# Optimization experiments

Measured on AMD Instinct MI355X. Metric: run time of the kernel, lower is better.

Reference implementation:

```python
import jax, jax.numpy as jnp
import numpy as np

N, E, IN_DIM, HID, HEADS, LAYERS, NTYPES, NGRAPH = 50000, 600000, 64, 128, 8, 3, 10, 500
C = HID // HEADS
NEG_SLOPE = 0.2
EPS = 1e-5


def setup_inputs() -> dict:
    key = jax.random.key(0)
    ks = jax.random.split(key, 24)
    inp = {
        "x": jax.random.normal(ks[0], (N, IN_DIM), jnp.float32),
        "edge_index": jax.random.randint(ks[1], (2, E), 0, N),
        "node_types": jax.random.randint(ks[2], (N,), 0, NTYPES),
        "batch": jnp.sort(jax.random.randint(ks[3], (N,), 0, NGRAPH)),
        # node embedding linear
        "emb_W": jax.random.normal(ks[4], (IN_DIM, HID), jnp.float32) / np.sqrt(IN_DIM),
        "emb_b": jnp.zeros((HID,), jnp.float32),
        "ntype_emb": jax.random.normal(ks[5], (NTYPES, HID), jnp.float32) * 0.02,
        # stacked GAT layer params
        "gat_W": jax.random.normal(ks[6], (LAYERS, HID, HID), jnp.float32) / np.sqrt(HID),
        "att_src": jax.random.normal(ks[7], (LAYERS, HEADS, C), jnp.float32) * 0.1,
        "att_dst": jax.random.normal(ks[8], (LAYERS, HEADS, C), jnp.float32) * 0.1,
        "gat_b": jnp.zeros((LAYERS, HID), jnp.float32),
        "ln_g": jnp.ones((LAYERS, HID), jnp.float32),
        "ln_b": jnp.zeros((LAYERS, HID), jnp.float32),
        # global attention MLP
        "ga_W1": jax.random.normal(ks[9], (HID, HID), jnp.float32) / np.sqrt(HID),
        "ga_b1": jnp.zeros((HID,), jnp.float32),
        "ga_W2": jax.random.normal(ks[10], (HID, 1), jnp.float32) / np.sqrt(HID),
        "ga_b2": jnp.zeros((1,), jnp.float32),
        # graph classifier head
        "cls_W1": jax.random.normal(ks[11], (HID, HID), jnp.float32) / np.sqrt(HID),
        "cls_b1": jnp.zeros((HID,), jnp.float32),
        "cls_W2": jax.random.normal(ks[12], (HID, 1), jnp.float32) / np.sqrt(HID),
        "cls_b2": jnp.zeros((1,), jnp.float32),
    }
    return inp


def _layer_norm(h, g, b):
    mu = jnp.mean(h, axis=-1, keepdims=True)
    var = jnp.mean(jnp.square(h - mu), axis=-1, keepdims=True)
    return (h - mu) * jax.lax.rsqrt(var + EPS) * g + b


def _gat_layer(h, src, dst, W, a_src, a_dst, bias):
    # h: [N, HID] -> per-head projection [N, H, C]
    hp = (h @ W).reshape(N, HEADS, C)
    alpha_s = jnp.sum(hp * a_src, axis=-1)  # [N, H]
    alpha_d = jnp.sum(hp * a_dst, axis=-1)  # [N, H]
    e = jax.nn.leaky_relu(alpha_s[src] + alpha_d[dst], NEG_SLOPE)  # [E', H]
    # segment softmax over incoming edges of each destination node
    m = jax.ops.segment_max(e, dst, num_segments=N)
    ex = jnp.exp(e - m[dst])
    s = jax.ops.segment_sum(ex, dst, num_segments=N)
    alpha = ex / s[dst]  # every node has a self-loop, so s > 0
    msg = hp[src] * alpha[:, :, None]  # [E', H, C]
    out = jax.ops.segment_sum(msg, dst, num_segments=N)  # [N, H, C]
    return out.reshape(N, HID) + bias


def reference(x, edge_index, node_types, batch, emb_W, emb_b, ntype_emb,
              gat_W, att_src, att_dst, gat_b, ln_g, ln_b,
              ga_W1, ga_b1, ga_W2, ga_b2, cls_W1, cls_b1, cls_W2, cls_b2):
    # self-loops (PyG GATConv add_self_loops=True)
    loop = jnp.arange(N)
    src = jnp.concatenate([edge_index[0], loop])
    dst = jnp.concatenate([edge_index[1], loop])

    h = x @ emb_W + emb_b
    h = h + ntype_emb[node_types]

    for l in range(LAYERS):
        h_prev = h
        h = _gat_layer(h, src, dst, gat_W[l], att_src[l], att_dst[l], gat_b[l])
        h = _layer_norm(h, ln_g[l], ln_b[l])
        h = jax.nn.relu(h + h_prev)

    # global attention pooling: softmax over all nodes (dim 0, as in source)
    scores = jnp.tanh(h @ ga_W1 + ga_b1) @ ga_W2 + ga_b2  # [N, 1]
    attw = jax.nn.softmax(scores, axis=0)
    h_graph = jnp.sum(h * attw, axis=0)  # [HID]

    # global mean pool per graph
    sums = jax.ops.segment_sum(h, batch, num_segments=NGRAPH)  # [G, HID]
    cnts = jax.ops.segment_sum(jnp.ones((N, 1), h.dtype), batch, num_segments=NGRAPH)
    mean_pool = sums / jnp.maximum(cnts, 1.0)

    hg = h_graph + mean_pool  # broadcast [HID] + [G, HID]

    # graph classifier head (features_batch=None path), squeeze(-1)
    out = jax.nn.relu(hg @ cls_W1 + cls_b1) @ cls_W2 + cls_b2
    return out.squeeze(-1)  # [G]
```

## Files before the change

### kernel.cpp

```cpp
#include <hip/hip_runtime.h>
#include <hip/hip_bf16.h>
#include <math.h>

#define HID 128
#define HEADS 8
#define INDIM 64

typedef _Float16 f16x8 __attribute__((ext_vector_type(8)));
typedef _Float16 f16x4 __attribute__((ext_vector_type(4)));
typedef _Float16 f16x2 __attribute__((ext_vector_type(2)));
typedef float f32x4 __attribute__((ext_vector_type(4)));

__device__ __forceinline__ float fast_tanh(float x) {
    return 1.f - 2.f / (__expf(2.f * x) + 1.f);
}

#if defined(__has_builtin)
#if __has_builtin(__builtin_amdgcn_fdot2)
#define HAVE_FDOT2 1
#endif
#endif

__global__ void prologue_kernel(const int* __restrict__ ei, int* __restrict__ deg,
                                const float* __restrict__ x, _Float16* __restrict__ x16,
                                const float* __restrict__ emb_W, const float* __restrict__ gat_W,
                                const float* __restrict__ ga_W1, _Float16* __restrict__ wt_emb,
                                _Float16* __restrict__ wt_gat, _Float16* __restrict__ wt_ga1,
                                const int* __restrict__ batch, int* __restrict__ gstart,
                                float* __restrict__ hgZ,
                                int E, int EE, int N, int G, int XT4) {
    int i = blockIdx.x * blockDim.x + threadIdx.x;
    if (i < XT4) {
        float4 v = ((const float4*)x)[i];
        f16x4 o; o[0] = (_Float16)v.x; o[1] = (_Float16)v.y; o[2] = (_Float16)v.z; o[3] = (_Float16)v.w;
        *(f16x4*)&x16[4 * i] = o;
    }
    if (i < EE) {
        int dst = (i < E) ? ei[E + i] : (i - E);
        atomicAdd(&deg[dst], 1);
    }
    if (i < 8192) {
        int k = i >> 7, n = i & 127;
        wt_emb[n * 64 + k] = (_Float16)emb_W[i];
    } else if (i < 8192 + 49152) {
        int j = i - 8192;
        int l = j >> 14, r = j & 16383;
        int k = r >> 7, n = r & 127;
        wt_gat[l * 16384 + n * 128 + k] = (_Float16)gat_W[j];
    } else if (i < 73728) {
        int j = i - 57344;
        int k = j >> 7, n = j & 127;
        wt_ga1[n * 128 + k] = (_Float16)ga_W1[j];
    } else if (i < 73728 + 129) {
        hgZ[i - 73728] = 0.f;
    }
    if (i >= 100000 && i - 100000 <= G) {
        int g = i - 100000;
        int lo = 0, hi = N;
        while (lo < hi) {
            int mid = (lo + hi) >> 1;
            if (batch[mid] < g) lo = mid + 1; else hi = mid;
        }
        gstart[g] = lo;
    }
}

__global__ void block_sum_kernel(const int* __restrict__ deg, int* __restrict__ partials, int N) {
    __shared__ int sdata[4];
    int t = threadIdx.x;
    int i = blockIdx.x * 256 + t;
    int v = (i < N) ? deg[i] : 0;
#pragma unroll
    for (int m = 32; m >= 1; m >>= 1) v += __shfl_xor(v, m, 64);
    if ((t & 63) == 0) sdata[t >> 6] = v;
    __syncthreads();
    if (t == 0) partials[blockIdx.x] = sdata[0] + sdata[1] + sdata[2] + sdata[3];
}

__global__ void scan_partials_kernel(int* __restrict__ partials, int nb) {
    int lane = threadIdx.x;
    int carry = 0;
    for (int base = 0; base < nb; base += 64) {
        int i = base + lane;
        int v = (i < nb) ? partials[i] : 0;
        int orig = v;
#pragma unroll
        for (int off = 1; off < 64; off <<= 1) {
            int x = __shfl_up(v, off, 64);
            if (lane >= off) v += x;
        }
        if (i < nb) partials[i] = v - orig + carry;
        carry += __shfl(v, 63, 64);
    }
}

__global__ void rowptr_kernel(const int* __restrict__ deg, const int* __restrict__ partials,
                              int* __restrict__ rowptr, int* __restrict__ woff, int N, int EE) {
    __shared__ int tmp[256];
    int t = threadIdx.x;
    int i = blockIdx.x * 256 + t;
    int v = (i < N) ? deg[i] : 0;
    tmp[t] = v;
    __syncthreads();
#pragma unroll
    for (int off = 1; off < 256; off <<= 1) {
        int x = (t >= off) ? tmp[t - off] : 0;
        __syncthreads();
        tmp[t] += x;
        __syncthreads();
    }
    int excl = tmp[t] - v + partials[blockIdx.x];
    if (i < N) { rowptr[i] = excl; woff[i] = excl; }
    if (blockIdx.x == 0 && t == 0) rowptr[N] = EE;
}

__global__ void scatter_kernel(const int* __restrict__ ei, int* __restrict__ woff,
                               int* __restrict__ esrc, int E, int EE) {
    int e = blockIdx.x * blockDim.x + threadIdx.x;
    if (e >= EE) return;
    int src, dst;
    if (e < E) { src = ei[e]; dst = ei[E + e]; } else { src = dst = e - E; }
    int slot = atomicAdd(&woff[dst], 1);
    esrc[slot] = src;
}

__global__ __launch_bounds__(256) void mfma_proj_kernel(
    int mode, int K, int N,
    const _Float16* __restrict__ A16, const _Float16* __restrict__ Wt,
    const float* __restrict__ bias, const float* __restrict__ nemb,
    const int* __restrict__ ntypes, _Float16* __restrict__ h16out,
    const float* __restrict__ asrc, const float* __restrict__ adst,
    _Float16* __restrict__ hp_out, float* __restrict__ als, float* __restrict__ ald,
    const float* __restrict__ w2, const float* __restrict__ b2,
    float* __restrict__ escore)
{
    __shared__ _Float16 w_lds[128 * 136];
    __shared__ _Float16 a_lds[64 * 136];
    int t = threadIdx.x;
    int KP = K + 8;
    int K8 = K >> 3;

    for (int i = t; i < 128 * K8; i += 256) {
        int row = i / K8, c8 = i - row * K8;
        *(f16x8*)&w_lds[row * KP + 8 * c8] = *(const f16x8*)&Wt[(size_t)row * K + 8 * c8];
    }

    int lane = t & 63, wv = t >> 6;
    int l15 = lane & 15, quad = lane >> 4;

    for (int tile = 0; tile < 2; ++tile) {
        int n0 = blockIdx.x * 128 + tile * 64;
        if (n0 >= N) break;
        __syncthreads();
        for (int i = t; i < 64 * K8; i += 256) {
            int row = i / K8, c8 = i - row * K8;
            f16x8 v = {};
            if (n0 + row < N) v = *(const f16x8*)&A16[(size_t)(n0 + row) * K + 8 * c8];
            *(f16x8*)&a_lds[row * KP + 8 * c8] = v;
        }
        __syncthreads();

        f32x4 acc[8];
#pragma unroll
        for (int c = 0; c < 8; ++c) acc[c] = (f32x4){0.f, 0.f, 0.f, 0.f};

        int ksteps = K >> 5;
        for (int kk = 0; kk < ksteps; ++kk) {
            f16x8 af = *(const f16x8*)&a_lds[(wv * 16 + l15) * KP + kk * 32 + quad * 8];
#pragma unroll
            for (int c = 0; c < 8; ++c) {
                f16x8 bf = *(const f16x8*)&w_lds[(c * 16 + l15) * KP + kk * 32 + quad * 8];
                acc[c] = __builtin_amdgcn_mfma_f32_16x16x32_f16(af, bf, acc[c], 0, 0, 0);
            }
        }

        if (mode == 0) {
            float bv[8];
#pragma unroll
            for (int c = 0; c < 8; ++c) bv[c] = bias[c * 16 + l15];
            __syncthreads();
#pragma unroll
            for (int r = 0; r < 4; ++r) {
                int n = n0 + wv * 16 + quad * 4 + r;
                int nt = (n < N) ? ntypes[n] : 0;
#pragma unroll
                for (int c = 0; c < 8; ++c)
                    a_lds[(wv * 16 + quad * 4 + r) * 136 + c * 16 + l15] =
                        (_Float16)(acc[c][r] + bv[c] + nemb[nt * HID + c * 16 + l15]);
            }
            __syncthreads();
            for (int i = t; i < 64 * 16; i += 256) {
                int row = i >> 4, c8 = i & 15;
                int n = n0 + row;
                if (n < N) *(f16x8*)&h16out[(size_t)n * HID + 8 * c8] = *(const f16x8*)&a_lds[row * 136 + 8 * c8];
            }
        } else if (mode == 1) {
            __syncthreads();
#pragma unroll
            for (int c = 0; c < 8; ++c)
#pragma unroll
                for (int r = 0; r < 4; ++r)
                    a_lds[(wv * 16 + quad * 4 + r) * 136 + c * 16 + l15] = (_Float16)acc[c][r];
            __syncthreads();
            for (int i = t; i < 64 * 16; i += 256) {
                int row = i >> 4, c8 = i & 15;
                int n = n0 + row;
                if (n < N) *(f16x8*)&hp_out[(size_t)n * HID + 8 * c8] = *(const f16x8*)&a_lds[row * 136 + 8 * c8];
            }
            for (int task = t; task < 512; task += 256) {
                int row = task >> 3, hd = task & 7;
                int n = n0 + row;
                if (n >= N) continue;
                f16x8 v0 = *(const f16x8*)&a_lds[row * 136 + hd * 16];
                f16x8 v1 = *(const f16x8*)&a_lds[row * 136 + hd * 16 + 8];
                float va = 0.f, vd = 0.f;
#pragma unroll
                for (int j = 0; j < 8; ++j) {
                    va += (float)v0[j] * asrc[hd * 16 + j] + (float)v1[j] * asrc[hd * 16 + 8 + j];
                    vd += (float)v0[j] * adst[hd * 16 + j] + (float)v1[j] * adst[hd * 16 + 8 + j];
                }
                als[n * HEADS + hd] = va;
                ald[n * HEADS + hd] = vd;
            }
        } else {
            float b2v = b2[0];
            float treg[4] = {0.f, 0.f, 0.f, 0.f};
#pragma unroll
            for (int c = 0; c < 8; ++c) {
                float b1v = bias[c * 16 + l15];
                float w2v = w2[c * 16 + l15];
#pragma unroll
                for (int r = 0; r < 4; ++r)
                    treg[r] += fast_tanh(acc[c][r] + b1v) * w2v;
            }
#pragma unroll
            for (int r = 0; r < 4; ++r) {
                float v = treg[r];
#pragma unroll
                for (int m = 8; m >= 1; m >>= 1) v += __shfl_xor(v, m, 64);
                if (l15 == 0) {
                    int n = n0 + wv * 16 + quad * 4 + r;
                    if (n < N) escore[n] = __expf(v + b2v);
                }
            }
        }
    }
}

__global__ void gat_aggregate_kernel(const int* __restrict__ rowptr, const int* __restrict__ esrc,
                                     const float* __restrict__ als, const float* __restrict__ ald,
                                     const _Float16* __restrict__ hp16, const float* __restrict__ gb,
                                     const float* __restrict__ lg, const float* __restrict__ lb,
                                     _Float16* __restrict__ h16, int N) {
    int wave = threadIdx.x >> 6;
    int lane = threadIdx.x & 63;
    int n = blockIdx.x * 4 + wave;
    if (n >= N) return;
    int esub = lane >> 4;
    int cg = lane & 15;
    int hd = cg >> 1;
    float adv = ald[n * HEADS + hd];
    int row = rowptr[n], end = rowptr[n + 1];
    int last = end - 1;
    float acc[8] = {0.f, 0.f, 0.f, 0.f, 0.f, 0.f, 0.f, 0.f};
    float sw = 0.f;
    for (int base = row; base < end; base += 16) {
        int iA = base + esub;
        int iB = iA + 4, iC = iA + 8, iD = iA + 12;
        int cA = iA <= last ? iA : last;
        int cB = iB <= last ? iB : last;
        int cC = iC <= last ? iC : last;
        int cD = iD <= last ? iD : last;
        int sA = esrc[cA], sB = esrc[cB], sC = esrc[cC], sD = esrc[cD];
        f16x8 pA = *(const f16x8*)&hp16[(size_t)sA * HID + cg * 8];
        f16x8 pB = *(const f16x8*)&hp16[(size_t)sB * HID + cg * 8];
        f16x8 pC = *(const f16x8*)&hp16[(size_t)sC * HID + cg * 8];
        f16x8 pD = *(const f16x8*)&hp16[(size_t)sD * HID + cg * 8];
        float aA = als[sA * HEADS + hd];
        float aB = als[sB * HEADS + hd];
        float aC = als[sC * HEADS + hd];
        float aD = als[sD * HEADS + hd];
        float lA = aA + adv; lA = lA > 0.f ? lA : 0.2f * lA;
        float lB = aB + adv; lB = lB > 0.f ? lB : 0.2f * lB;
        float lC = aC + adv; lC = lC > 0.f ? lC : 0.2f * lC;
        float lD = aD + adv; lD = lD > 0.f ? lD : 0.2f * lD;
        float wA = __expf(lA) * ((iA < end) ? 1.f : 0.f);
        float wB = __expf(lB) * ((iB < end) ? 1.f : 0.f);
        float wC = __expf(lC) * ((iC < end) ? 1.f : 0.f);
        float wD = __expf(lD) * ((iD < end) ? 1.f : 0.f);
        sw += (wA + wB) + (wC + wD);
#ifdef HAVE_FDOT2
        f16x2 wAB; wAB[0] = (_Float16)wA; wAB[1] = (_Float16)wB;
        f16x2 wCD; wCD[0] = (_Float16)wC; wCD[1] = (_Float16)wD;
#pragma unroll
        for (int j = 0; j < 8; ++j) {
            f16x2 prAB; prAB[0] = pA[j]; prAB[1] = pB[j];
            f16x2 prCD; prCD[0] = pC[j]; prCD[1] = pD[j];
            acc[j] = __builtin_amdgcn_fdot2(prAB, wAB, acc[j], false);
            acc[j] = __builtin_amdgcn_fdot2(prCD, wCD, acc[j], false);
        }
#else
#pragma unroll
        for (int j = 0; j < 8; ++j)
            acc[j] += wA * (float)pA[j] + wB * (float)pB[j]
                    + wC * (float)pC[j] + wD * (float)pD[j];
#endif
    }
#pragma unroll
    for (int m = 16; m <= 32; m <<= 1) {
        sw += __shfl_xor(sw, m, 64);
#pragma unroll
        for (int j = 0; j < 8; ++j) acc[j] += __shfl_xor(acc[j], m, 64);
    }
    float inv_sw = 1.f / sw;
    float4 g0 = ((const float4*)(gb + cg * 8))[0];
    float4 g1 = ((const float4*)(gb + cg * 8))[1];
    float v[8];
    v[0] = acc[0] * inv_sw + g0.x; v[1] = acc[1] * inv_sw + g0.y;
    v[2] = acc[2] * inv_sw + g0.z; v[3] = acc[3] * inv_sw + g0.w;
    v[4] = acc[4] * inv_sw + g1.x; v[5] = acc[5] * inv_sw + g1.y;
    v[6] = acc[6] * inv_sw + g1.z; v[7] = acc[7] * inv_sw + g1.w;
    float s = 0.f;
#pragma unroll
    for (int j = 0; j < 8; ++j) s += v[j];
#pragma unroll
    for (int m = 32; m >= 1; m >>= 1) s += __shfl_xor(s, m, 64);
    float mu = s * (1.f / 512.f);
    float d[8], sq = 0.f;
#pragma unroll
    for (int j = 0; j < 8; ++j) { d[j] = v[j] - mu; sq += d[j] * d[j]; }
#pragma unroll
    for (int m = 32; m >= 1; m >>= 1) sq += __shfl_xor(sq, m, 64);
    float inv = rsqrtf(sq * (1.f / 512.f) + 1e-5f);
    float4 lg0 = ((const float4*)(lg + cg * 8))[0];
    float4 lg1 = ((const float4*)(lg + cg * 8))[1];
    float4 lb0 = ((const float4*)(lb + cg * 8))[0];
    float4 lb1 = ((const float4*)(lb + cg * 8))[1];
    float lgv[8] = {lg0.x, lg0.y, lg0.z, lg0.w, lg1.x, lg1.y, lg1.z, lg1.w};
    float lbv[8] = {lb0.x, lb0.y, lb0.z, lb0.w, lb1.x, lb1.y, lb1.z, lb1.w};
    f16x8 hold = *(const f16x8*)&h16[(size_t)n * HID + cg * 8];
    f16x8 hnew;
#pragma unroll
    for (int j = 0; j < 8; ++j) {
        float r = d[j] * inv * lgv[j] + lbv[j] + (float)hold[j];
        hnew[j] = (_Float16)(r > 0.f ? r : 0.f);
    }
    if (esub == 0) *(f16x8*)&h16[(size_t)n * HID + cg * 8] = hnew;
}

__global__ void pool_graph_kernel(const _Float16* __restrict__ h16, const float* __restrict__ escore,
                                  const int* __restrict__ gstart, float* __restrict__ sums,
                                  float* __restrict__ cnts, float* __restrict__ hgZ, int G) {
    int g = blockIdx.x;
    int t = threadIdx.x;
    int c = t & 127, grp = t >> 7;
    int s = gstart[g], e = gstart[g + 1];
    float msum = 0.f, asum = 0.f, z = 0.f;
    for (int n = s + grp; n < e; n += 4) {
        float hv = (float)h16[(size_t)n * HID + c];
        float es = escore[n];
        msum += hv;
        asum += es * hv;
        if (c == 0) z += es;
    }
    __shared__ float sm[4][HID];
    __shared__ float sa[4][HID];
    __shared__ float sz[4];
    sm[grp][c] = msum;
    sa[grp][c] = asum;
    if (c == 0) sz[grp] = z;
    __syncthreads();
    if (t < HID) {
        float m = sm[0][t] + sm[1][t] + sm[2][t] + sm[3][t];
        float a = sa[0][t] + sa[1][t] + sa[2][t] + sa[3][t];
        sums[(size_t)g * HID + t] = m;
        atomicAdd(&hgZ[t], a);
    } else if (t == HID) {
        cnts[g] = (float)(e - s);
        atomicAdd(&hgZ[HID], sz[0] + sz[1] + sz[2] + sz[3]);
    }
}

__global__ void head_kernel(const float* __restrict__ hgZ, const float* __restrict__ sums,
                            const float* __restrict__ cnts, const float* __restrict__ W1,
                            const float* __restrict__ b1, const float* __restrict__ W2,
                            const float* __restrict__ b2, float* __restrict__ out, int G) {
    int g = blockIdx.x;
    int t = threadIdx.x;
    __shared__ float hr[HID];
    __shared__ float part[2];
    float Z = hgZ[HID];
    float cnt = cnts[g];
    cnt = cnt > 1.f ? cnt : 1.f;
    hr[t] = hgZ[t] / Z + sums[(size_t)g * HID + t] / cnt;
    __syncthreads();
    float acc = b1[t];
#pragma unroll 8
    for (int k = 0; k < HID; ++k) acc += hr[k] * W1[k * HID + t];
    acc = acc > 0.f ? acc : 0.f;
    float v = acc * W2[t];
#pragma unroll
    for (int m = 32; m >= 1; m >>= 1) v += __shfl_xor(v, m, 64);
    if ((t & 63) == 0) part[t >> 6] = v;
    __syncthreads();
    if (t == 0) out[g] = part[0] + part[1] + b2[0];
}

extern "C" void kernel_launch(void* const* d_in, const int* in_sizes, int n_in,
                              void* d_out, int out_size, void* d_ws, size_t ws_size,
                              hipStream_t stream) {
    const float* x        = (const float*)d_in[0];
    const int*   ei       = (const int*)d_in[1];
    const int*   ntypes   = (const int*)d_in[2];
    const int*   batch    = (const int*)d_in[3];
    const float* emb_W    = (const float*)d_in[4];
    const float* emb_b    = (const float*)d_in[5];
    const float* nemb     = (const float*)d_in[6];
    const float* gat_W    = (const float*)d_in[7];
    const float* att_src  = (const float*)d_in[8];
    const float* att_dst  = (const float*)d_in[9];
    const float* gat_b    = (const float*)d_in[10];
    const float* ln_g     = (const float*)d_in[11];
    const float* ln_b     = (const float*)d_in[12];
    const float* ga_W1    = (const float*)d_in[13];
    const float* ga_b1    = (const float*)d_in[14];
    const float* ga_W2    = (const float*)d_in[15];
    const float* ga_b2    = (const float*)d_in[16];
    const float* cls_W1   = (const float*)d_in[17];
    const float* cls_b1   = (const float*)d_in[18];
    const float* cls_W2   = (const float*)d_in[19];
    const float* cls_b2   = (const float*)d_in[20];
    float* out = (float*)d_out;

    const int N  = in_sizes[2];
    const int E  = in_sizes[1] / 2;
    const int EE = E + N;
    const int G  = out_size;
    const int NB = (N + 255) / 256;
    const int XT4 = N * INDIM / 4;

    float* ws      = (float*)d_ws;
    float* als     = ws;
    float* ald     = als + (size_t)N * HEADS;
    float* escore  = ald + (size_t)N * HEADS;
    float* sums    = escore + N;
    float* cnts    = sums + (size_t)G * HID;
    float* hgZ     = cnts + G;
    _Float16* h16  = (_Float16*)(hgZ + HID + 1);
    _Float16* hp16 = h16 + (size_t)N * HID;
    _Float16* x16  = hp16 + (size_t)N * HID;
    _Float16* wt_emb = x16 + (size_t)N * INDIM;
    _Float16* wt_gat = wt_emb + 128 * 64;
    _Float16* wt_ga1 = wt_gat + 3 * 128 * 128;
    int*   rowptr  = (int*)(wt_ga1 + 128 * 128);
    int*   woff    = rowptr + (N + 1);
    int*   deg     = woff + N;
    int*   esrc    = deg + N;
    int*   partials= esrc + EE;
    int*   gstart  = partials + NB;

    hipMemsetAsync(deg, 0, (size_t)N * sizeof(int), stream);
    int ptot = XT4 > EE ? XT4 : EE;
    if (ptot < 100000 + G + 1) ptot = 100000 + G + 1;
    prologue_kernel<<<(ptot + 255) / 256, 256, 0, stream>>>(
        ei, deg, x, x16, emb_W, gat_W, ga_W1, wt_emb, wt_gat, wt_ga1,
        batch, gstart, hgZ, E, EE, N, G, XT4);
    block_sum_kernel<<<NB, 256, 0, stream>>>(deg, partials, N);
    scan_partials_kernel<<<1, 64, 0, stream>>>(partials, NB);
    rowptr_kernel<<<NB, 256, 0, stream>>>(deg, partials, rowptr, woff, N, EE);
    scatter_kernel<<<(EE + 255) / 256, 256, 0, stream>>>(ei, woff, esrc, E, EE);

    const int PB = (N + 127) / 128;

    mfma_proj_kernel<<<PB, 256, 0, stream>>>(
        0, INDIM, N, x16, wt_emb, emb_b, nemb, ntypes, h16,
        nullptr, nullptr, nullptr, nullptr, nullptr, nullptr, nullptr, nullptr);

    for (int l = 0; l < 3; ++l) {
        mfma_proj_kernel<<<PB, 256, 0, stream>>>(
            1, HID, N, h16, wt_gat + (size_t)l * HID * HID,
            nullptr, nullptr, nullptr, nullptr,
            att_src + l * HID, att_dst + l * HID,
            hp16, als, ald, nullptr, nullptr, nullptr);
        gat_aggregate_kernel<<<(N + 3) / 4, 256, 0, stream>>>(
            rowptr, esrc, als, ald, hp16,
            gat_b + l * HID, ln_g + l * HID, ln_b + l * HID, h16, N);
    }

    mfma_proj_kernel<<<PB, 256, 0, stream>>>(
        2, HID, N, h16, wt_ga1, ga_b1, nullptr, nullptr, nullptr,
        nullptr, nullptr, nullptr, nullptr, nullptr, ga_W2, ga_b2, escore);

    pool_graph_kernel<<<G, 512, 0, stream>>>(h16, escore, gstart, sums, cnts, hgZ, G);
    head_kernel<<<G, 128, 0, stream>>>(hgZ, sums, cnts, cls_W1, cls_b1, cls_W2, cls_b2, out, G);
}
```

Before: 405.7 us.

## Fuse CSR build into projection kernels and compute block partials via atomics

Per-block degree partials are now accumulated with atomics in the prologue, spread over four slots per block to reduce contention. This removes the separate block-sum and partial-scan kernels. The rowptr scan runs as extra blocks appended to the embedding projection launch, and the edge scatter runs as extra blocks appended to the first GAT projection launch, so CSR construction overlaps with MFMA work and four launches disappear. Each rowptr block now sums all preceding partials itself, which costs redundant reads, and the prologue adds a second atomic per edge.

Measured after the change: 529.0 us. 30.4% more time.

```diff
diff --git a/kernel.cpp b/kernel.cpp
--- a/kernel.cpp
+++ b/kernel.cpp
@@ -22,6 +22,7 @@
 #endif
 
 __global__ void prologue_kernel(const int* __restrict__ ei, int* __restrict__ deg,
+                                int* __restrict__ partials,
                                 const float* __restrict__ x, _Float16* __restrict__ x16,
                                 const float* __restrict__ emb_W, const float* __restrict__ gat_W,
                                 const float* __restrict__ ga_W1, _Float16* __restrict__ wt_emb,
@@ -38,6 +39,7 @@
     if (i < EE) {
         int dst = (i < E) ? ei[E + i] : (i - E);
         atomicAdd(&deg[dst], 1);
+        atomicAdd(&partials[((dst >> 8) << 2) | (i & 3)], 1);
     }
     if (i < 8192) {
         int k = i >> 7, n = i & 127;
@@ -65,65 +67,6 @@
     }
 }
 
-__global__ void block_sum_kernel(const int* __restrict__ deg, int* __restrict__ partials, int N) {
-    __shared__ int sdata[4];
-    int t = threadIdx.x;
-    int i = blockIdx.x * 256 + t;
-    int v = (i < N) ? deg[i] : 0;
-#pragma unroll
-    for (int m = 32; m >= 1; m >>= 1) v += __shfl_xor(v, m, 64);
-    if ((t & 63) == 0) sdata[t >> 6] = v;
-    __syncthreads();
-    if (t == 0) partials[blockIdx.x] = sdata[0] + sdata[1] + sdata[2] + sdata[3];
-}
-
-__global__ void scan_partials_kernel(int* __restrict__ partials, int nb) {
-    int lane = threadIdx.x;
-    int carry = 0;
-    for (int base = 0; base < nb; base += 64) {
-        int i = base + lane;
-        int v = (i < nb) ? partials[i] : 0;
-        int orig = v;
-#pragma unroll
-        for (int off = 1; off < 64; off <<= 1) {
-            int x = __shfl_up(v, off, 64);
-            if (lane >= off) v += x;
-        }
-        if (i < nb) partials[i] = v - orig + carry;
-        carry += __shfl(v, 63, 64);
-    }
-}
-
-__global__ void rowptr_kernel(const int* __restrict__ deg, const int* __restrict__ partials,
-                              int* __restrict__ rowptr, int* __restrict__ woff, int N, int EE) {
-    __shared__ int tmp[256];
-    int t = threadIdx.x;
-    int i = blockIdx.x * 256 + t;
-    int v = (i < N) ? deg[i] : 0;
-    tmp[t] = v;
-    __syncthreads();
-#pragma unroll
-    for (int off = 1; off < 256; off <<= 1) {
-        int x = (t >= off) ? tmp[t - off] : 0;
-        __syncthreads();
-        tmp[t] += x;
-        __syncthreads();
-    }
-    int excl = tmp[t] - v + partials[blockIdx.x];
-    if (i < N) { rowptr[i] = excl; woff[i] = excl; }
-    if (blockIdx.x == 0 && t == 0) rowptr[N] = EE;
-}
-
-__global__ void scatter_kernel(const int* __restrict__ ei, int* __restrict__ woff,
-                               int* __restrict__ esrc, int E, int EE) {
-    int e = blockIdx.x * blockDim.x + threadIdx.x;
-    if (e >= EE) return;
-    int src, dst;
-    if (e < E) { src = ei[e]; dst = ei[E + e]; } else { src = dst = e - E; }
-    int slot = atomicAdd(&woff[dst], 1);
-    esrc[slot] = src;
-}
-
 __global__ __launch_bounds__(256) void mfma_proj_kernel(
     int mode, int K, int N,
     const _Float16* __restrict__ A16, const _Float16* __restrict__ Wt,
@@ -132,11 +75,55 @@
     const float* __restrict__ asrc, const float* __restrict__ adst,
     _Float16* __restrict__ hp_out, float* __restrict__ als, float* __restrict__ ald,
     const float* __restrict__ w2, const float* __restrict__ b2,
-    float* __restrict__ escore)
+    float* __restrict__ escore,
+    int PB, int task, const int* __restrict__ ei2,
+    const int* __restrict__ degc, const int* __restrict__ partialsc,
+    int* __restrict__ rowptrw, int* __restrict__ woffw, int* __restrict__ esrcw,
+    int E2, int EE2)
 {
     __shared__ _Float16 w_lds[128 * 136];
     __shared__ _Float16 a_lds[64 * 136];
     int t = threadIdx.x;
+
+    if ((int)blockIdx.x >= PB) {
+        if (task == 1) {
+            int* itmp  = (int*)a_lds;
+            int* itmp2 = itmp + 256;
+            int b = (int)blockIdx.x - PB;
+            int i = b * 256 + t;
+            int v = (i < N) ? degc[i] : 0;
+            itmp[t] = v;
+            __syncthreads();
+#pragma unroll
+            for (int off = 1; off < 256; off <<= 1) {
+                int x = (t >= off) ? itmp[t - off] : 0;
+                __syncthreads();
+                itmp[t] += x;
+                __syncthreads();
+            }
+            int pe = 0;
+            for (int j = t; j < (b << 2); j += 256) pe += partialsc[j];
+#pragma unroll
+            for (int m = 32; m >= 1; m >>= 1) pe += __shfl_xor(pe, m, 64);
+            if ((t & 63) == 0) itmp2[t >> 6] = pe;
+            __syncthreads();
+            pe = itmp2[0] + itmp2[1] + itmp2[2] + itmp2[3];
+            int excl = itmp[t] - v + pe;
+            if (i < N) { rowptrw[i] = excl; woffw[i] = excl; }
+            if (b == 0 && t == 0) rowptrw[N] = EE2;
+        } else {
+            int sb = (int)blockIdx.x - PB;
+            int stride = ((int)gridDim.x - PB) << 8;
+            for (int e = sb * 256 + t; e < EE2; e += stride) {
+                int src, dst;
+                if (e < E2) { src = ei2[e]; dst = ei2[E2 + e]; } else { src = dst = e - E2; }
+                int slot = atomicAdd(&woffw[dst], 1);
+                esrcw[slot] = src;
+            }
+        }
+        return;
+    }
+
     int KP = K + 8;
     int K8 = K >> 3;
 
@@ -207,8 +194,8 @@
                 int n = n0 + row;
                 if (n < N) *(f16x8*)&hp_out[(size_t)n * HID + 8 * c8] = *(const f16x8*)&a_lds[row * 136 + 8 * c8];
             }
-            for (int task = t; task < 512; task += 256) {
-                int row = task >> 3, hd = task & 7;
+            for (int task2 = t; task2 < 512; task2 += 256) {
+                int row = task2 >> 3, hd = task2 & 7;
                 int n = n0 + row;
                 if (n >= N) continue;
                 f16x8 v0 = *(const f16x8*)&a_lds[row * 136 + hd * 16];
@@ -455,33 +442,43 @@
     int*   rowptr  = (int*)(wt_ga1 + 128 * 128);
     int*   woff    = rowptr + (N + 1);
     int*   deg     = woff + N;
-    int*   esrc    = deg + N;
-    int*   partials= esrc + EE;
-    int*   gstart  = partials + NB;
-
-    hipMemsetAsync(deg, 0, (size_t)N * sizeof(int), stream);
+    int*   partials= deg + N;
+    int*   esrc    = partials + 4 * NB;
+    int*   gstart  = esrc + EE;
+
+    hipMemsetAsync(deg, 0, ((size_t)N + 4 * (size_t)NB) * sizeof(int), stream);
     int ptot = XT4 > EE ? XT4 : EE;
     if (ptot < 100000 + G + 1) ptot = 100000 + G + 1;
     prologue_kernel<<<(ptot + 255) / 256, 256, 0, stream>>>(
-        ei, deg, x, x16, emb_W, gat_W, ga_W1, wt_emb, wt_gat, wt_ga1,
+        ei, deg, partials, x, x16, emb_W, gat_W, ga_W1, wt_emb, wt_gat, wt_ga1,
         batch, gstart, hgZ, E, EE, N, G, XT4);
-    block_sum_kernel<<<NB, 256, 0, stream>>>(deg, partials, N);
-    scan_partials_kernel<<<1, 64, 0, stream>>>(partials, NB);
-    rowptr_kernel<<<NB, 256, 0, stream>>>(deg, partials, rowptr, woff, N, EE);
-    scatter_kernel<<<(EE + 255) / 256, 256, 0, stream>>>(ei, woff, esrc, E, EE);
 
     const int PB = (N + 127) / 128;
-
-    mfma_proj_kernel<<<PB, 256, 0, stream>>>(
+    int SCB = 768 - PB;
+    if (SCB < 128) SCB = 128;
+
+    mfma_proj_kernel<<<PB + NB, 256, 0, stream>>>(
         0, INDIM, N, x16, wt_emb, emb_b, nemb, ntypes, h16,
-        nullptr, nullptr, nullptr, nullptr, nullptr, nullptr, nullptr, nullptr);
-
-    for (int l = 0; l < 3; ++l) {
+        nullptr, nullptr, nullptr, nullptr, nullptr, nullptr, nullptr, nullptr,
+        PB, 1, nullptr, deg, partials, rowptr, woff, nullptr, E, EE);
+
+    mfma_proj_kernel<<<PB + SCB, 256, 0, stream>>>(
+        1, HID, N, h16, wt_gat,
+        nullptr, nullptr, nullptr, nullptr,
+        att_src, att_dst, hp16, als, ald, nullptr, nullptr, nullptr,
+        PB, 2, ei, nullptr, nullptr, nullptr, woff, esrc, E, EE);
+
+    gat_aggregate_kernel<<<(N + 3) / 4, 256, 0, stream>>>(
+        rowptr, esrc, als, ald, hp16,
+        gat_b, ln_g, ln_b, h16, N);
+
+    for (int l = 1; l < 3; ++l) {
         mfma_proj_kernel<<<PB, 256, 0, stream>>>(
             1, HID, N, h16, wt_gat + (size_t)l * HID * HID,
             nullptr, nullptr, nullptr, nullptr,
             att_src + l * HID, att_dst + l * HID,
-            hp16, als, ald, nullptr, nullptr, nullptr);
+            hp16, als, ald, nullptr, nullptr, nullptr,
+            PB, 0, nullptr, nullptr, nullptr, nullptr, nullptr, nullptr, 0, 0);
         gat_aggregate_kernel<<<(N + 3) / 4, 256, 0, stream>>>(
             rowptr, esrc, als, ald, hp16,
             gat_b + l * HID, ln_g + l * HID, ln_b + l * HID, h16, N);
@@ -489,7 +486,8 @@
 
     mfma_proj_kernel<<<PB, 256, 0, stream>>>(
         2, HID, N, h16, wt_ga1, ga_b1, nullptr, nullptr, nullptr,
-        nullptr, nullptr, nullptr, nullptr, nullptr, ga_W2, ga_b2, escore);
+        nullptr, nullptr, nullptr, nullptr, nullptr, ga_W2, ga_b2, escore,
+        PB, 0, nullptr, nullptr, nullptr, nullptr, nullptr, nullptr, 0, 0);
 
     pool_graph_kernel<<<G, 512, 0, stream>>>(h16, escore, gstart, sums, cnts, hgZ, G);
     head_kernel<<<G, 128, 0, stream>>>(hgZ, sums, cnts, cls_W1, cls_b1, cls_W2, cls_b2, out, G);
```
